# Kernel optimization log

Measured on AMD Instinct MI355X. Metric: run time of the kernel, lower is better.

## Reference

```python
import jax, jax.numpy as jnp
import numpy as np

EMPHASIS_FACTOR = 1.5

def setup_inputs() -> dict:
    key = jax.random.key(0)
    k1, k2 = jax.random.split(key)
    B, T, F = 32, 4096, 256
    x = jax.random.normal(k1, (B, T, F), dtype=jnp.float32)
    W = jax.random.normal(k2, (F, 1), dtype=jnp.float32) * (1.0 / np.sqrt(F))
    b = jnp.zeros((1,), dtype=jnp.float32)
    return {"x": x, "W": W, "b": b}

def reference(x, W, b):
    # x: [B, T, F], W: [F, 1], b: [1]
    B, T, F = x.shape
    e = jnp.tanh(x @ W + b)                 # [B, T, 1]
    a = jax.nn.softmax(e, axis=1)           # softmax over time
    a_flat = a[..., 0]                      # [B, T]
    k = max(1, int(T * 0.1))
    _, top_idx = jax.lax.top_k(a_flat, k)   # [B, k]
    # scatter True at top-k positions (instead of O(T*k) broadcast compare)
    mask = jnp.zeros((B, T), dtype=bool).at[jnp.arange(B)[:, None], top_idx].set(True)
    a_emph = jnp.where(mask[..., None], a * EMPHASIS_FACTOR, a)  # [B, T, 1]
    return jnp.sum(x * a_emph, axis=1, keepdims=True)            # [B, 1, F]
```

## Files before the change

### kernel.cpp

```cpp
#include <hip/hip_runtime.h>
#include <math.h>

#define BB 32
#define TT 4096
#define FF 256
#define CH 64
#define NC (TT / CH)
#define K_TOP 409
#define EMPH_HALF 0.5f
#define NSEG 16
#define SEGT (TT / NSEG)
#define CPS (NC / NSEG)

__device__ __forceinline__ unsigned flip_key(float v) {
    unsigned u = __float_as_uint(v);
    return (u & 0x80000000u) ? ~u : (u | 0x80000000u);
}
__device__ __forceinline__ float unflip_key(unsigned k) {
    unsigned u = (k & 0x80000000u) ? (k & 0x7fffffffu) : ~k;
    return __uint_as_float(u);
}
__device__ __forceinline__ float fast_tanh(float z) {
    z = fminf(fmaxf(z, -15.f), 15.f);
    const float t = __expf(2.f * z);
    return (t - 1.f) * __builtin_amdgcn_rcpf(t + 1.f);
}

__global__ __launch_bounds__(256) void fused_pass1(const float* __restrict__ x,
                                                   const float* __restrict__ W,
                                                   const float* __restrict__ bias,
                                                   float* __restrict__ e,
                                                   float* __restrict__ P,
                                                   float* __restrict__ cm,
                                                   float* __restrict__ cs) {
    const int b = blockIdx.x / NC;
    const int c = blockIdx.x % NC;
    const int tid = threadIdx.x;
    const int wv = tid >> 6, ln = tid & 63;

    const float* xc = x + ((size_t)b * TT + (size_t)c * CH) * FF;
    const float4 wvec = ((const float4*)W)[ln];
    const float  bb   = bias[0];

    float4 acc = make_float4(0.f, 0.f, 0.f, 0.f);
    float  m = -1e30f, ssum = 0.f;

    #pragma unroll
    for (int s0 = 0; s0 < CH; s0 += 16) {
        const int r0 = s0 + wv * 4;
        float4 xr[4];
        #pragma unroll
        for (int i = 0; i < 4; i++)
            xr[i] = ((const float4*)(xc + (size_t)(r0 + i) * FF))[ln];

        float dv[4];
        #pragma unroll
        for (int i = 0; i < 4; i++)
            dv[i] = xr[i].x * wvec.x + xr[i].y * wvec.y +
                    xr[i].z * wvec.z + xr[i].w * wvec.w;
        #pragma unroll
        for (int i = 0; i < 4; i++) {
            float d = dv[i];
            #pragma unroll
            for (int off = 32; off; off >>= 1) d += __shfl_xor(d, off);
            dv[i] = fast_tanh(d + bb);
        }
        if (ln == 0)
            *(float4*)(e + (size_t)b * TT + c * CH + r0) =
                make_float4(dv[0], dv[1], dv[2], dv[3]);

        float lm = m;
        #pragma unroll
        for (int i = 0; i < 4; i++) lm = fmaxf(lm, dv[i]);
        const float alpha = __expf(m - lm);
        acc.x *= alpha; acc.y *= alpha; acc.z *= alpha; acc.w *= alpha;
        ssum *= alpha;
        #pragma unroll
        for (int i = 0; i < 4; i++) {
            const float wgt = __expf(dv[i] - lm);
            ssum += wgt;
            acc.x += wgt * xr[i].x; acc.y += wgt * xr[i].y;
            acc.z += wgt * xr[i].z; acc.w += wgt * xr[i].w;
        }
        m = lm;
    }

    __shared__ float4 part4[4][64];
    __shared__ float sm[4], ss4[4];
    part4[wv][ln] = acc;
    if (ln == 0) { sm[wv] = m; ss4[wv] = ssum; }
    __syncthreads();

    const float m0 = sm[0], m1 = sm[1], m2 = sm[2], m3 = sm[3];
    const float mc = fmaxf(fmaxf(m0, m1), fmaxf(m2, m3));
    const float s0s = __expf(m0 - mc), s1s = __expf(m1 - mc);
    const float s2s = __expf(m2 - mc), s3s = __expf(m3 - mc);
    const float* pf = (const float*)part4;
    const float p = pf[tid] * s0s + pf[256 + tid] * s1s +
                    pf[512 + tid] * s2s + pf[768 + tid] * s3s;
    P[((size_t)b * NC + c) * FF + tid] = p;
    if (tid == 0) {
        cm[b * NC + c] = mc;
        cs[b * NC + c] = ss4[0] * s0s + ss4[1] * s1s + ss4[2] * s2s + ss4[3] * s3s;
    }
}

__global__ __launch_bounds__(256) void select_kernel(const float* __restrict__ e,
                                                     const float* __restrict__ cm,
                                                     const float* __restrict__ cs,
                                                     float* __restrict__ stats,
                                                     float* __restrict__ out) {
    const int b = blockIdx.x;
    const int tid = threadIdx.x;
    const int wv = tid >> 6, ln = tid & 63;

    out[b * FF + tid] = 0.f;

    __shared__ float sgm, sZ;
    __shared__ int   sc4[4];

    if (tid < 64) {
        const float mm = cm[b * NC + tid];
        const float ss = cs[b * NC + tid];
        float g = mm;
        #pragma unroll
        for (int off = 32; off; off >>= 1) g = fmaxf(g, __shfl_xor(g, off));
        float zz = ss * __expf(mm - g);
        #pragma unroll
        for (int off = 32; off; off >>= 1) zz += __shfl_xor(zz, off);
        if (tid == 0) { sgm = g; sZ = zz; }
    }

    const float* eb = e + (size_t)b * TT;
    unsigned key[16];
    #pragma unroll
    for (int j = 0; j < 16; j++) key[j] = flip_key(eb[tid + 256 * j]);

    unsigned prefix = 0u, mask = 0u;
    int kk = K_TOP;
    for (int bit = 31; bit >= 0; bit--) {
        const unsigned bm = 1u << bit;
        const unsigned m2 = mask | bm;
        const unsigned want = prefix | bm;
        int cnt = 0;
        #pragma unroll
        for (int j = 0; j < 16; j++)
            cnt += (int)__popcll(__ballot((key[j] & m2) == want));
        __syncthreads();
        if (ln == 0) sc4[wv] = cnt;
        __syncthreads();
        const int tot = sc4[0] + sc4[1] + sc4[2] + sc4[3];
        if (tot >= kk) prefix = want; else kk -= tot;
        mask = m2;
    }

    if (tid == 0) {
        stats[3 * b + 0] = sgm;
        stats[3 * b + 1] = sZ;
        stats[3 * b + 2] = __uint_as_float(prefix);
    }
}

__global__ __launch_bounds__(256) void combine_kernel(const float* __restrict__ x,
                                                      const float* __restrict__ e,
                                                      const float* __restrict__ P,
                                                      const float* __restrict__ cm,
                                                      const float* __restrict__ stats,
                                                      float* __restrict__ out) {
    const int b = blockIdx.x / NSEG;
    const int s = blockIdx.x % NSEG;
    const int tid = threadIdx.x;

    const float gmax = stats[3 * b + 0];
    const float Z    = stats[3 * b + 1];
    const unsigned Kkey = __float_as_uint(stats[3 * b + 2]);

    float acc = 0.f;
    #pragma unroll
    for (int c = 0; c < CPS; c++) {
        const int cc = s * CPS + c;
        const float sc2 = __expf(cm[b * NC + cc] - gmax);
        acc += P[((size_t)b * NC + cc) * FF + tid] * sc2;
    }

    __shared__ int scount;
    __shared__ int slist[SEGT];
    __shared__ float sval[SEGT];
    if (tid == 0) scount = 0;
    __syncthreads();

    const int t = s * SEGT + tid;
    const float ev = e[(size_t)b * TT + t];
    if (flip_key(ev) >= Kkey) {
        const int i = atomicAdd(&scount, 1);
        slist[i] = t;
        sval[i] = EMPH_HALF * __expf(ev - gmax);
    }
    __syncthreads();

    const int n = scount;
    const float* xb = x + (size_t)b * TT * FF;
    for (int i = 0; i < n; i++)
        acc += sval[i] * xb[(size_t)slist[i] * FF + tid];

    atomicAdd(&out[b * FF + tid], acc * (1.f / Z));
}

extern "C" void kernel_launch(void* const* d_in, const int* in_sizes, int n_in,
                              void* d_out, int out_size, void* d_ws, size_t ws_size,
                              hipStream_t stream) {
    const float* x    = (const float*)d_in[0];
    const float* W    = (const float*)d_in[1];
    const float* bias = (const float*)d_in[2];
    float* out = (float*)d_out;

    float* e     = (float*)d_ws;
    float* P     = e + (size_t)BB * TT;
    float* cm    = P + (size_t)BB * NC * FF;
    float* cs    = cm + BB * NC;
    float* stats = cs + BB * NC;

    fused_pass1<<<BB * NC, 256, 0, stream>>>(x, W, bias, e, P, cm, cs);
    select_kernel<<<BB, 256, 0, stream>>>(e, cm, cs, stats, out);
    combine_kernel<<<BB * NSEG, 256, 0, stream>>>(x, e, P, cm, stats, out);
}
```

Baseline: 209.9 us.

## Cut select-kernel barriers, add early exit, widen combine grid and unroll gathers

The radix-select loop now uses a double-buffered shared count array, so it needs one barrier per bit instead of two. It also stops early once the count exactly matches the remaining k. Keys are loaded as float4, the softmax stats stay in registers instead of shared memory, and zeroing of the output moves into the first kernel. The combine kernel uses twice as many segments with half-sized time slices, and its gather of emphasized rows is unrolled by four to get more loads in flight. The cost is more atomic adds to the output and a thread guard in the combine kernel.

```diff
diff --git a/kernel.cpp b/kernel.cpp
--- a/kernel.cpp
+++ b/kernel.cpp
@@ -8,17 +8,13 @@
 #define NC (TT / CH)
 #define K_TOP 409
 #define EMPH_HALF 0.5f
-#define NSEG 16
+#define NSEG 32
 #define SEGT (TT / NSEG)
 #define CPS (NC / NSEG)
 
 __device__ __forceinline__ unsigned flip_key(float v) {
     unsigned u = __float_as_uint(v);
     return (u & 0x80000000u) ? ~u : (u | 0x80000000u);
-}
-__device__ __forceinline__ float unflip_key(unsigned k) {
-    unsigned u = (k & 0x80000000u) ? (k & 0x7fffffffu) : ~k;
-    return __uint_as_float(u);
 }
 __device__ __forceinline__ float fast_tanh(float z) {
     z = fminf(fmaxf(z, -15.f), 15.f);
@@ -32,11 +28,14 @@
                                                    float* __restrict__ e,
                                                    float* __restrict__ P,
                                                    float* __restrict__ cm,
-                                                   float* __restrict__ cs) {
+                                                   float* __restrict__ cs,
+                                                   float* __restrict__ out) {
     const int b = blockIdx.x / NC;
     const int c = blockIdx.x % NC;
     const int tid = threadIdx.x;
     const int wv = tid >> 6, ln = tid & 63;
+
+    if (c == 0) out[b * FF + tid] = 0.f;
 
     const float* xc = x + ((size_t)b * TT + (size_t)c * CH) * FF;
     const float4 wvec = ((const float4*)W)[ln];
@@ -108,36 +107,38 @@
 __global__ __launch_bounds__(256) void select_kernel(const float* __restrict__ e,
                                                      const float* __restrict__ cm,
                                                      const float* __restrict__ cs,
-                                                     float* __restrict__ stats,
-                                                     float* __restrict__ out) {
+                                                     float* __restrict__ stats) {
     const int b = blockIdx.x;
     const int tid = threadIdx.x;
     const int wv = tid >> 6, ln = tid & 63;
 
-    out[b * FF + tid] = 0.f;
-
-    __shared__ float sgm, sZ;
-    __shared__ int   sc4[4];
-
+    float g = 0.f, zz = 0.f;
     if (tid < 64) {
         const float mm = cm[b * NC + tid];
         const float ss = cs[b * NC + tid];
-        float g = mm;
+        g = mm;
         #pragma unroll
         for (int off = 32; off; off >>= 1) g = fmaxf(g, __shfl_xor(g, off));
-        float zz = ss * __expf(mm - g);
+        zz = ss * __expf(mm - g);
         #pragma unroll
         for (int off = 32; off; off >>= 1) zz += __shfl_xor(zz, off);
-        if (tid == 0) { sgm = g; sZ = zz; }
-    }
-
-    const float* eb = e + (size_t)b * TT;
+    }
+
+    const float4* eb4 = (const float4*)(e + (size_t)b * TT);
     unsigned key[16];
     #pragma unroll
-    for (int j = 0; j < 16; j++) key[j] = flip_key(eb[tid + 256 * j]);
-
+    for (int j = 0; j < 4; j++) {
+        const float4 v = eb4[tid + 256 * j];
+        key[4 * j + 0] = flip_key(v.x);
+        key[4 * j + 1] = flip_key(v.y);
+        key[4 * j + 2] = flip_key(v.z);
+        key[4 * j + 3] = flip_key(v.w);
+    }
+
+    __shared__ int sc[2][4];
     unsigned prefix = 0u, mask = 0u;
     int kk = K_TOP;
+    int pb = 0;
     for (int bit = 31; bit >= 0; bit--) {
         const unsigned bm = 1u << bit;
         const unsigned m2 = mask | bm;
@@ -146,17 +147,22 @@
         #pragma unroll
         for (int j = 0; j < 16; j++)
             cnt += (int)__popcll(__ballot((key[j] & m2) == want));
+        if (ln == 0) sc[pb][wv] = cnt;
         __syncthreads();
-        if (ln == 0) sc4[wv] = cnt;
-        __syncthreads();
-        const int tot = sc4[0] + sc4[1] + sc4[2] + sc4[3];
-        if (tot >= kk) prefix = want; else kk -= tot;
+        const int tot = sc[pb][0] + sc[pb][1] + sc[pb][2] + sc[pb][3];
+        pb ^= 1;
+        if (tot >= kk) {
+            prefix = want;
+            if (tot == kk) break;
+        } else {
+            kk -= tot;
+        }
         mask = m2;
     }
 
     if (tid == 0) {
-        stats[3 * b + 0] = sgm;
-        stats[3 * b + 1] = sZ;
+        stats[3 * b + 0] = g;
+        stats[3 * b + 1] = zz;
         stats[3 * b + 2] = __uint_as_float(prefix);
     }
 }
@@ -189,18 +195,30 @@
     if (tid == 0) scount = 0;
     __syncthreads();
 
-    const int t = s * SEGT + tid;
-    const float ev = e[(size_t)b * TT + t];
-    if (flip_key(ev) >= Kkey) {
-        const int i = atomicAdd(&scount, 1);
-        slist[i] = t;
-        sval[i] = EMPH_HALF * __expf(ev - gmax);
+    if (tid < SEGT) {
+        const int t = s * SEGT + tid;
+        const float ev = e[(size_t)b * TT + t];
+        if (flip_key(ev) >= Kkey) {
+            const int i = atomicAdd(&scount, 1);
+            slist[i] = t;
+            sval[i] = EMPH_HALF * __expf(ev - gmax);
+        }
     }
     __syncthreads();
 
     const int n = scount;
     const float* xb = x + (size_t)b * TT * FF;
-    for (int i = 0; i < n; i++)
+    int i = 0;
+    for (; i + 4 <= n; i += 4) {
+        const float* p0 = xb + (size_t)slist[i + 0] * FF;
+        const float* p1 = xb + (size_t)slist[i + 1] * FF;
+        const float* p2 = xb + (size_t)slist[i + 2] * FF;
+        const float* p3 = xb + (size_t)slist[i + 3] * FF;
+        const float w0 = sval[i + 0], w1 = sval[i + 1];
+        const float w2 = sval[i + 2], w3 = sval[i + 3];
+        acc += w0 * p0[tid] + w1 * p1[tid] + w2 * p2[tid] + w3 * p3[tid];
+    }
+    for (; i < n; i++)
         acc += sval[i] * xb[(size_t)slist[i] * FF + tid];
 
     atomicAdd(&out[b * FF + tid], acc * (1.f / Z));
@@ -220,7 +238,7 @@
     float* cs    = cm + BB * NC;
     float* stats = cs + BB * NC;
 
-    fused_pass1<<<BB * NC, 256, 0, stream>>>(x, W, bias, e, P, cm, cs);
-    select_kernel<<<BB, 256, 0, stream>>>(e, cm, cs, stats, out);
+    fused_pass1<<<BB * NC, 256, 0, stream>>>(x, W, bias, e, P, cm, cs, out);
+    select_kernel<<<BB, 256, 0, stream>>>(e, cm, cs, stats);
     combine_kernel<<<BB * NSEG, 256, 0, stream>>>(x, e, P, cm, stats, out);
 }
```

After: 207.3 us. No clear change (-1.2%).
